# Optimization experiments

Measured on AMD Instinct MI355X. Metric: run time of the kernel, lower is better.

Reference implementation:

```python
import jax, jax.numpy as jnp
import numpy as np

L, B, T, V, E, H = 6, 4, 1024, 32000, 768, 12
D = E // H  # head_size = 64


def setup_inputs() -> dict:
    key = jax.random.key(0)
    ks = jax.random.split(key, 12)
    s = 0.02
    n = lambda k, shape: jax.random.normal(k, shape, jnp.float32) * s
    return {
        "idx": jax.random.randint(ks[0], (B, T), 0, V),
        "tok_emb": n(ks[1], (V, E)),
        "pos_emb": n(ks[2], (T, E)),
        "ln1_w": jnp.ones((L, E)), "ln1_b": jnp.zeros((L, E)),
        "wq": n(ks[3], (L, E, H, D)),
        "wk": n(ks[4], (L, E, H, D)),
        "wv": n(ks[5], (L, E, H, D)),
        "wo": n(ks[6], (L, E, E)), "bo": jnp.zeros((L, E)),
        "ln2_w": jnp.ones((L, E)), "ln2_b": jnp.zeros((L, E)),
        "w1": n(ks[7], (L, E, 4 * E)), "b1": jnp.zeros((L, 4 * E)),
        "w2": n(ks[8], (L, 4 * E, E)), "b2": jnp.zeros((L, E)),
        "lnf_w": jnp.ones((E,)), "lnf_b": jnp.zeros((E,)),
        "head_w": n(ks[9], (E, V)), "head_b": jnp.zeros((V,)),
    }


def _ln(x, w, b, eps=1e-5):
    m = x.mean(-1, keepdims=True)
    v = ((x - m) ** 2).mean(-1, keepdims=True)
    return (x - m) * jax.lax.rsqrt(v + eps) * w + b


def _forward(idx, tok_emb, pos_emb, ln1_w, ln1_b, wq, wk, wv, wo, bo,
             ln2_w, ln2_b, w1, b1, w2, b2, lnf_w, lnf_b, head_w, head_b):
    t = idx.shape[1]
    x = tok_emb[idx] + pos_emb[None, :t]          # [B,T,E]
    causal = jnp.tril(jnp.ones((t, t), bool))     # tril buffer
    scale = jnp.asarray(D, x.dtype) ** -0.5       # k.shape[-1] ** -0.5

    def block(x, p):
        l1w, l1b, Wq, Wk, Wv, Wo, Bo, l2w, l2b, W1, B1, W2, B2 = p
        h = _ln(x, l1w, l1b)
        q = jnp.einsum('btc,chd->bthd', h, Wq)
        k = jnp.einsum('btc,chd->bthd', h, Wk)
        v = jnp.einsum('btc,chd->bthd', h, Wv)
        wei = jnp.einsum('bqhd,bkhd->bhqk', q, k) * scale
        wei = jnp.where(causal, wei, -jnp.inf)
        wei = jax.nn.softmax(wei, axis=-1)
        att = jnp.einsum('bhqk,bkhd->bqhd', wei, v).reshape(x.shape)
        x = x + (att @ Wo + Bo)
        h2 = _ln(x, l2w, l2b)
        x = x + (jax.nn.relu(h2 @ W1 + B1) @ W2 + B2)
        return x, None

    params = (ln1_w, ln1_b, wq, wk, wv, wo, bo, ln2_w, ln2_b, w1, b1, w2, b2)
    x, _ = jax.lax.scan(block, x, params)
    x = _ln(x, lnf_w, lnf_b)
    return x @ head_w + head_b                    # [B,T,V] logits


def reference(idx, tok_emb, pos_emb, ln1_w, ln1_b, wq, wk, wv, wo, bo,
              ln2_w, ln2_b, w1, b1, w2, b2, lnf_w, lnf_b, head_w, head_b):
    return _forward(idx, tok_emb, pos_emb, ln1_w, ln1_b, wq, wk, wv, wo, bo,
                    ln2_w, ln2_b, w1, b1, w2, b2, lnf_w, lnf_b, head_w, head_b)
```

## Files before the change

### kernel.cpp

```cpp
#include <hip/hip_runtime.h>
#include <hip/hip_bf16.h>
#include <math.h>

#define L_LAYERS 6
#define BB 4
#define TT 1024
#define VV 32000
#define EE 768
#define HH 12
#define DD 64
#define BT (BB * TT)

typedef unsigned short u16;
typedef unsigned int   u32;
typedef __attribute__((ext_vector_type(8))) short short8;
typedef __attribute__((ext_vector_type(8))) unsigned short ushort8v;
typedef __attribute__((ext_vector_type(4))) float f32x4;

__device__ __forceinline__ float b2f_lo(u32 u) { union { u32 i; float f; } c; c.i = u << 16;          return c.f; }
__device__ __forceinline__ float b2f_hi(u32 u) { union { u32 i; float f; } c; c.i = u & 0xffff0000u;  return c.f; }
__device__ __forceinline__ u16  f2b(float f)   { union { float f; u32 i; } c{f}; u32 r = c.i + 0x7fffu + ((c.i >> 16) & 1u); return (u16)(r >> 16); }

__device__ __forceinline__ void gload16(const void* g, void* l) {
    __builtin_amdgcn_global_load_lds(
        (const __attribute__((address_space(1))) void*)g,
        (__attribute__((address_space(3))) void*)l, 16, 0, 0);
}

__global__ __launch_bounds__(256) void embed_kernel(
    const int* __restrict__ idx, const float* __restrict__ tok_emb,
    const float* __restrict__ pos_emb, float* __restrict__ x)
{
    int i = blockIdx.x * 256 + threadIdx.x;
    int e  = i % EE;
    int bt = i / EE;
    int t  = bt % TT;
    int tok = idx[bt];
    x[i] = tok_emb[(size_t)tok * EE + e] + pos_emb[(size_t)t * EE + e];
}

__global__ __launch_bounds__(256) void ln_kernel(
    const float* __restrict__ X, const float* __restrict__ w,
    const float* __restrict__ b, u16* __restrict__ Y)
{
    const int tid = threadIdx.x;
    const size_t row = blockIdx.x;
    const float* x = X + row * EE;

    float v0 = x[tid], v1 = x[tid + 256], v2 = x[tid + 512];

    __shared__ float red[256];
    red[tid] = v0 + v1 + v2;
    __syncthreads();
    for (int off = 128; off > 0; off >>= 1) {
        if (tid < off) red[tid] += red[tid + off];
        __syncthreads();
    }
    float mean = red[0] * (1.0f / EE);
    __syncthreads();
    float d0 = v0 - mean, d1 = v1 - mean, d2 = v2 - mean;
    red[tid] = d0 * d0 + d1 * d1 + d2 * d2;
    __syncthreads();
    for (int off = 128; off > 0; off >>= 1) {
        if (tid < off) red[tid] += red[tid + off];
        __syncthreads();
    }
    float rstd = rsqrtf(red[0] * (1.0f / EE) + 1e-5f);

    u16* y = Y + row * EE;
    y[tid]       = f2b(d0 * rstd * w[tid]       + b[tid]);
    y[tid + 256] = f2b(d1 * rstd * w[tid + 256] + b[tid + 256]);
    y[tid + 512] = f2b(d2 * rstd * w[tid + 512] + b[tid + 512]);
}

__device__ __forceinline__ void transpose_tile(
    const float* __restrict__ W, u16* __restrict__ Wt,
    int K, int N, int kt, int nt)
{
    __shared__ float t[32][33];
    const int k0 = kt * 32;
    const int n0 = nt * 32;
    const int c = threadIdx.x & 31;
    const int r = threadIdx.x >> 5;
    #pragma unroll
    for (int i = 0; i < 4; i++)
        t[r + i * 8][c] = W[(size_t)(k0 + r + i * 8) * N + n0 + c];
    __syncthreads();
    #pragma unroll
    for (int i = 0; i < 4; i++) {
        int rr = r + i * 8;
        Wt[(size_t)(n0 + rr) * K + k0 + c] = f2b(t[c][rr]);
    }
}

__global__ __launch_bounds__(256) void transpose_cvt(
    const float* __restrict__ W, u16* __restrict__ Wt, int K, int N)
{
    transpose_tile(W, Wt, K, N, blockIdx.y, blockIdx.x);
}

__global__ __launch_bounds__(256) void transpose_layer(
    const float* __restrict__ wq, const float* __restrict__ wk,
    const float* __restrict__ wv, const float* __restrict__ wo,
    const float* __restrict__ w1, const float* __restrict__ w2,
    u16* __restrict__ wt)
{
    const int t = blockIdx.x;
    if (t < 2304) {
        const int m = t / 576, r = t % 576;
        const float* Ws[4] = {wq, wk, wv, wo};
        transpose_tile(Ws[m], wt + (size_t)m * 768 * 768, 768, 768, r / 24, r % 24);
    } else if (t < 4608) {
        const int r = t - 2304;
        transpose_tile(w1, wt + (size_t)4 * 768 * 768, 768, 3072, r / 96, r % 96);
    } else {
        const int r = t - 4608;
        transpose_tile(w2, wt + (size_t)4 * 768 * 768 + (size_t)3072 * 768,
                       3072, 768, r / 24, r % 24);
    }
}

template<int RELU, int RES, int OUTBF, int MFRAG, int VECST>
__global__ __launch_bounds__(256) void gemm_bf16(
    const u16* __restrict__ A, const u16* __restrict__ Bt,
    const float* __restrict__ bias, const float* __restrict__ res,
    void* __restrict__ Cv, int M, int N, int K)
{
    constexpr int TM = MFRAG * 32;
    __shared__ u16 SH[(TM + 128) * 64];
    u16* As = SH;
    u16* Bs = SH + TM * 64;

    const int tid  = threadIdx.x;
    const int lane = tid & 63;
    const int w    = tid >> 6;
    const int wr   = w >> 1, wc = w & 1;
    const int m0 = blockIdx.x * TM;
    const int n0 = blockIdx.y * 128;

    const int cs = (lane & 7) ^ (lane >> 3);
    const int rl = lane >> 3;

    int aoff[2 * MFRAG], boff[8];
    const int kq = lane >> 4;
    #pragma unroll
    for (int mi = 0; mi < MFRAG; mi++) {
        int rg = wr * (MFRAG * 16) + mi * 16 + (lane & 15);
        #pragma unroll
        for (int ks = 0; ks < 2; ks++)
            aoff[2 * mi + ks] = rg * 64 + (((ks * 4 + kq) ^ (rg & 7)) * 8);
    }
    #pragma unroll
    for (int ni = 0; ni < 4; ni++) {
        int rg = wc * 64 + ni * 16 + (lane & 15);
        #pragma unroll
        for (int ks = 0; ks < 2; ks++)
            boff[2 * ni + ks] = rg * 64 + (((ks * 4 + kq) ^ (rg & 7)) * 8);
    }

    f32x4 acc[MFRAG][4] = {};

    for (int k0 = 0; k0 < K; k0 += 64) {
        __syncthreads();
        #pragma unroll
        for (int i = 0; i < MFRAG; i++) {
            const int seg = i * 4 + w;
            const int row = seg * 8 + rl;
            gload16(A + (size_t)(m0 + row) * K + k0 + cs * 8, &As[seg * 512]);
        }
        #pragma unroll
        for (int i = 0; i < 4; i++) {
            const int seg = i * 4 + w;
            const int row = seg * 8 + rl;
            gload16(Bt + (size_t)(n0 + row) * K + k0 + cs * 8, &Bs[seg * 512]);
        }
        __syncthreads();
        #pragma unroll
        for (int ks = 0; ks < 2; ks++) {
            short8 af[MFRAG], bfv[4];
            #pragma unroll
            for (int mi = 0; mi < MFRAG; mi++) af[mi] = *(const short8*)&As[aoff[2 * mi + ks]];
            #pragma unroll
            for (int ni = 0; ni < 4; ni++) bfv[ni] = *(const short8*)&Bs[boff[2 * ni + ks]];
            #pragma unroll
            for (int mi = 0; mi < MFRAG; mi++)
                #pragma unroll
                for (int ni = 0; ni < 4; ni++)
                    acc[mi][ni] = __builtin_amdgcn_mfma_f32_16x16x32_bf16(
                        af[mi], bfv[ni], acc[mi][ni], 0, 0, 0);
        }
    }

    const int rbase = m0 + wr * (MFRAG * 16) + (lane >> 4) * 4;
    const int cbase = n0 + wc * 64 + (lane & 15);

    if (VECST) {
        __syncthreads();
        float* CF = (float*)SH;
        #pragma unroll
        for (int ch = 0; ch < 2; ++ch) {
            if (wr == ch) {
                #pragma unroll
                for (int ni = 0; ni < 4; ni++) {
                    const int c = cbase + ni * 16;
                    const float bvf = bias ? bias[c] : 0.0f;
                    #pragma unroll
                    for (int mi = 0; mi < MFRAG; mi++)
                        #pragma unroll
                        for (int i = 0; i < 4; i++)
                            CF[(mi * 16 + kq * 4 + i) * 128 + wc * 64 + ni * 16 + (lane & 15)]
                                = acc[mi][ni][i] + bvf;
                }
            }
            __syncthreads();
            const int rr = tid >> 5;
            const int cc = (tid & 31) * 4;
            #pragma unroll
            for (int j = 0; j < 8; ++j) {
                const int r = rr + j * 8;
                *(f32x4*)&((float*)Cv)[(size_t)(m0 + ch * 64 + r) * N + n0 + cc]
                    = *(const f32x4*)&CF[r * 128 + cc];
            }
            if (ch == 0) __syncthreads();
        }
    } else {
        #pragma unroll
        for (int ni = 0; ni < 4; ni++) {
            const int c = cbase + ni * 16;
            const float bv = bias ? bias[c] : 0.0f;
            #pragma unroll
            for (int mi = 0; mi < MFRAG; mi++) {
                const int r = rbase + mi * 16;
                #pragma unroll
                for (int i = 0; i < 4; i++) {
                    float v = acc[mi][ni][i] + bv;
                    const size_t off = (size_t)(r + i) * N + c;
                    if (RES)  v += res[off];
                    if (RELU) v = fmaxf(v, 0.0f);
                    if (OUTBF) ((u16*)Cv)[off] = f2b(v);
                    else       ((float*)Cv)[off] = v;
                }
            }
        }
    }
}

#define AST 72
__global__ __launch_bounds__(256) void attn_mfma(
    const u16* __restrict__ qkv, u16* __restrict__ O)
{
    const int tid = threadIdx.x;
    const int qi = blockIdx.x;
    const int h  = blockIdx.y;
    const int b  = blockIdx.z;
    const int q0 = qi * 64;

    __shared__ u16 Ks[2][64 * 64];
    __shared__ u16 Vt[2][64 * AST];
    __shared__ u16 Ps[64 * AST];

    const int lane = tid & 63;
    const int w    = tid >> 6;
    const int lr   = lane & 15;
    const int lk   = lane >> 4;

    const int cs = (lane & 7) ^ (lane >> 3);
    const int rl = lane >> 3;
    const int vk2 = tid & 31;
    const int vdc = tid >> 5;

    {
        const int sr = tid >> 2, sc = tid & 3;
        const u16* src = qkv + (size_t)(b * TT + q0 + sr) * 2304 + h * 64 + sc * 16;
        *(ushort8v*)&Ps[sr * AST + sc * 16]     = *(const ushort8v*)src;
        *(ushort8v*)&Ps[sr * AST + sc * 16 + 8] = *(const ushort8v*)(src + 8);
    }
    __syncthreads();
    short8 aq[2];
    #pragma unroll
    for (int ks = 0; ks < 2; ks++)
        aq[ks] = *(const short8*)&Ps[(w * 16 + lr) * AST + lk * 8 + ks * 32];

    ushort8v vr0, vr1;
    auto K_ISSUE = [&](int t, int bf) {
        const int k0 = t * 64;
        #pragma unroll
        for (int j = 0; j < 2; ++j) {
            const int seg = j * 4 + w;
            const int row = seg * 8 + rl;
            gload16(qkv + (size_t)(b * TT + k0 + row) * 2304 + 768 + h * 64 + cs * 8,
                    &Ks[bf][seg * 512]);
        }
    };
    auto V_LOAD = [&](int t) {
        const int k0 = t * 64;
        const u16* p = qkv + (size_t)(b * TT + k0 + 2 * vk2) * 2304 + 1536 + h * 64 + vdc * 8;
        vr0 = *(const ushort8v*)p;
        vr1 = *(const ushort8v*)(p + 2304);
    };
    auto V_WRITE = [&](int bf) {
        #pragma unroll
        for (int j = 0; j < 8; ++j) {
            const u32 val = (u32)vr0[j] | ((u32)vr1[j] << 16);
            *(u32*)&Vt[bf][(vdc * 8 + j) * AST + 2 * vk2] = val;
        }
    };

    K_ISSUE(0, 0);
    V_LOAD(0);
    V_WRITE(0);
    __syncthreads();

    f32x4 oacc[4] = {};
    float m_run[4], l_run[4];
    #pragma unroll
    for (int i = 0; i < 4; i++) { m_run[i] = -3.0e38f; l_run[i] = 0.0f; }

    const int qrow = q0 + w * 16 + lk * 4;

    for (int t = 0; t <= qi; ++t) {
        const int cur = t & 1;

        f32x4 sfrag[4] = {};
        #pragma unroll
        for (int ks = 0; ks < 2; ks++)
            #pragma unroll
            for (int nt = 0; nt < 4; nt++) {
                const int rg = nt * 16 + lr;
                short8 bk = *(const short8*)&Ks[cur][rg * 64 + (((ks * 4 + lk) ^ (rg & 7)) * 8)];
                sfrag[nt] = __builtin_amdgcn_mfma_f32_16x16x32_bf16(aq[ks], bk, sfrag[nt], 0, 0, 0);
            }

        if (t < qi) { K_ISSUE(t + 1, cur ^ 1); V_LOAD(t + 1); }

        const int k0 = t * 64;
        float sv[4][4], mxv[4];
        float need = 0.0f;
        #pragma unroll
        for (int i = 0; i < 4; i++) {
            float mx = -3.0e38f;
            #pragma unroll
            for (int nt = 0; nt < 4; nt++) {
                float s = sfrag[nt][i] * 0.125f;
                if (t == qi && (k0 + nt * 16 + lr) > (qrow + i)) s = -3.0e38f;
                sv[i][nt] = s;
                mx = fmaxf(mx, s);
            }
            mx = fmaxf(mx, __shfl_xor(mx, 1));
            mx = fmaxf(mx, __shfl_xor(mx, 2));
            mx = fmaxf(mx, __shfl_xor(mx, 4));
            mx = fmaxf(mx, __shfl_xor(mx, 8));
            mxv[i] = mx;
            need = fmaxf(need, mx - m_run[i]);
        }
        if (!__all(need <= 8.0f)) {
            #pragma unroll
            for (int i = 0; i < 4; i++) {
                const float m_new = fmaxf(m_run[i], mxv[i]);
                const float scale = __expf(m_run[i] - m_new);
                l_run[i] *= scale;
                #pragma unroll
                for (int dt = 0; dt < 4; dt++) oacc[dt][i] *= scale;
                m_run[i] = m_new;
            }
        }
        #pragma unroll
        for (int i = 0; i < 4; i++) {
            float rs = 0.0f;
            #pragma unroll
            for (int nt = 0; nt < 4; nt++) {
                const float p = __expf(sv[i][nt] - m_run[i]);
                sv[i][nt] = p;
                rs += p;
            }
            rs += __shfl_xor(rs, 1);
            rs += __shfl_xor(rs, 2);
            rs += __shfl_xor(rs, 4);
            rs += __shfl_xor(rs, 8);
            l_run[i] += rs;
        }

        #pragma unroll
        for (int i = 0; i < 4; i++)
            #pragma unroll
            for (int nt = 0; nt < 4; nt++)
                Ps[(w * 16 + lk * 4 + i) * AST + nt * 16 + lr] = f2b(sv[i][nt]);

        #pragma unroll
        for (int ks = 0; ks < 2; ks++) {
            short8 ap = *(const short8*)&Ps[(w * 16 + lr) * AST + lk * 8 + ks * 32];
            #pragma unroll
            for (int dt = 0; dt < 4; dt++) {
                short8 bv = *(const short8*)&Vt[cur][(dt * 16 + lr) * AST + lk * 8 + ks * 32];
                oacc[dt] = __builtin_amdgcn_mfma_f32_16x16x32_bf16(ap, bv, oacc[dt], 0, 0, 0);
            }
        }

        if (t < qi) V_WRITE(cur ^ 1);
        __syncthreads();
    }

    #pragma unroll
    for (int i = 0; i < 4; i++) {
        const float inv = 1.0f / l_run[i];
        u16* dst = O + (size_t)(b * TT + q0 + w * 16 + lk * 4 + i) * 768 + h * 64 + lr;
        #pragma unroll
        for (int dt = 0; dt < 4; dt++)
            dst[dt * 16] = f2b(oacc[dt][i] * inv);
    }
}

extern "C" void kernel_launch(void* const* d_in, const int* in_sizes, int n_in,
                              void* d_out, int out_size, void* d_ws, size_t ws_size,
                              hipStream_t stream)
{
    (void)in_sizes; (void)n_in; (void)out_size; (void)ws_size;

    const int*   idx     = (const int*)  d_in[0];
    const float* tok_emb = (const float*)d_in[1];
    const float* pos_emb = (const float*)d_in[2];
    const float* ln1_w   = (const float*)d_in[3];
    const float* ln1_b   = (const float*)d_in[4];
    const float* wq      = (const float*)d_in[5];
    const float* wk      = (const float*)d_in[6];
    const float* wv      = (const float*)d_in[7];
    const float* wo      = (const float*)d_in[8];
    const float* bo      = (const float*)d_in[9];
    const float* ln2_w   = (const float*)d_in[10];
    const float* ln2_b   = (const float*)d_in[11];
    const float* w1      = (const float*)d_in[12];
    const float* b1      = (const float*)d_in[13];
    const float* w2      = (const float*)d_in[14];
    const float* b2      = (const float*)d_in[15];
    const float* lnf_w   = (const float*)d_in[16];
    const float* lnf_b   = (const float*)d_in[17];
    const float* head_w  = (const float*)d_in[18];
    const float* head_b  = (const float*)d_in[19];
    float* out = (float*)d_out;

    const size_t S = (size_t)BT * EE;
    float* x   = (float*)d_ws;
    u16*  qkv  = (u16*)(x + S);
    u16*  hb   = qkv + (size_t)BT * 2304;
    u16*  ffh  = hb + S;
    u16*  wt   = ffh + (size_t)BT * 3072;

    embed_kernel<<<BT * EE / 256, 256, 0, stream>>>(idx, tok_emb, pos_emb, x);

    for (int l = 0; l < L_LAYERS; l++) {
        const size_t oE  = (size_t)l * EE;
        const size_t oEE = (size_t)l * EE * EE;
        const size_t oEF = (size_t)l * EE * 4 * EE;

        transpose_layer<<<6912, 256, 0, stream>>>(
            wq + oEE, wk + oEE, wv + oEE, wo + oEE, w1 + oEF, w2 + oEF, wt);

        ln_kernel<<<BT, 256, 0, stream>>>(x, ln1_w + oE, ln1_b + oE, hb);
        gemm_bf16<0, 0, 1, 4, 0><<<dim3(BT / 128, 2304 / 128), 256, 0, stream>>>(
            hb, wt, nullptr, nullptr, qkv, BT, 2304, 768);
        attn_mfma<<<dim3(TT / 64, HH, BB), 256, 0, stream>>>(qkv, hb);
        gemm_bf16<0, 1, 0, 2, 0><<<dim3(BT / 64, 768 / 128), 256, 0, stream>>>(
            hb, wt + (size_t)3 * 768 * 768, bo + oE, x, x, BT, 768, 768);
        ln_kernel<<<BT, 256, 0, stream>>>(x, ln2_w + oE, ln2_b + oE, hb);
        gemm_bf16<1, 0, 1, 4, 0><<<dim3(BT / 128, 3072 / 128), 256, 0, stream>>>(
            hb, wt + (size_t)4 * 768 * 768, b1 + (size_t)l * 4 * EE, nullptr, ffh, BT, 3072, 768);
        gemm_bf16<0, 1, 0, 2, 0><<<dim3(BT / 64, 768 / 128), 256, 0, stream>>>(
            ffh, wt + (size_t)4 * 768 * 768 + (size_t)3072 * 768, b2 + oE, x, x, BT, 768, 3072);
    }

    ln_kernel<<<BT, 256, 0, stream>>>(x, lnf_w, lnf_b, hb);
    transpose_cvt<<<dim3(VV / 32, EE / 32), 256, 0, stream>>>(head_w, wt, EE, VV);
    gemm_bf16<0, 0, 0, 4, 1><<<dim3(BT / 128, VV / 128), 256, 0, stream>>>(
        hb, wt, head_b, nullptr, out, BT, VV, 768);
}
```

Baseline: 1.532 ms.

## Use wave-per-row layernorm, XCD-aware GEMM tile swizzle, exp2 softmax, drop staged store

```diff
diff --git a/kernel.cpp b/kernel.cpp
--- a/kernel.cpp
+++ b/kernel.cpp
@@ -15,6 +15,7 @@
 typedef unsigned int   u32;
 typedef __attribute__((ext_vector_type(8))) short short8;
 typedef __attribute__((ext_vector_type(8))) unsigned short ushort8v;
+typedef __attribute__((ext_vector_type(4))) unsigned short ushort4v;
 typedef __attribute__((ext_vector_type(4))) float f32x4;
 
 __device__ __forceinline__ float b2f_lo(u32 u) { union { u32 i; float f; } c; c.i = u << 16;          return c.f; }
@@ -43,34 +44,44 @@
     const float* __restrict__ X, const float* __restrict__ w,
     const float* __restrict__ b, u16* __restrict__ Y)
 {
-    const int tid = threadIdx.x;
-    const size_t row = blockIdx.x;
+    const int lane = threadIdx.x & 63;
+    const size_t row = blockIdx.x * 4 + (threadIdx.x >> 6);
     const float* x = X + row * EE;
 
-    float v0 = x[tid], v1 = x[tid + 256], v2 = x[tid + 512];
-
-    __shared__ float red[256];
-    red[tid] = v0 + v1 + v2;
-    __syncthreads();
-    for (int off = 128; off > 0; off >>= 1) {
-        if (tid < off) red[tid] += red[tid + off];
-        __syncthreads();
-    }
-    float mean = red[0] * (1.0f / EE);
-    __syncthreads();
-    float d0 = v0 - mean, d1 = v1 - mean, d2 = v2 - mean;
-    red[tid] = d0 * d0 + d1 * d1 + d2 * d2;
-    __syncthreads();
-    for (int off = 128; off > 0; off >>= 1) {
-        if (tid < off) red[tid] += red[tid + off];
-        __syncthreads();
-    }
-    float rstd = rsqrtf(red[0] * (1.0f / EE) + 1e-5f);
+    f32x4 v[3];
+    #pragma unroll
+    for (int k = 0; k < 3; k++)
+        v[k] = *(const f32x4*)&x[lane * 4 + k * 256];
+
+    float s = 0.0f;
+    #pragma unroll
+    for (int k = 0; k < 3; k++) s += v[k][0] + v[k][1] + v[k][2] + v[k][3];
+    #pragma unroll
+    for (int off = 32; off; off >>= 1) s += __shfl_xor(s, off);
+    const float mean = s * (1.0f / EE);
+
+    float q = 0.0f;
+    #pragma unroll
+    for (int k = 0; k < 3; k++)
+        #pragma unroll
+        for (int j = 0; j < 4; j++) {
+            v[k][j] -= mean;
+            q += v[k][j] * v[k][j];
+        }
+    #pragma unroll
+    for (int off = 32; off; off >>= 1) q += __shfl_xor(q, off);
+    const float rstd = rsqrtf(q * (1.0f / EE) + 1e-5f);
 
     u16* y = Y + row * EE;
-    y[tid]       = f2b(d0 * rstd * w[tid]       + b[tid]);
-    y[tid + 256] = f2b(d1 * rstd * w[tid + 256] + b[tid + 256]);
-    y[tid + 512] = f2b(d2 * rstd * w[tid + 512] + b[tid + 512]);
+    #pragma unroll
+    for (int k = 0; k < 3; k++) {
+        const f32x4 wv = *(const f32x4*)&w[lane * 4 + k * 256];
+        const f32x4 bv = *(const f32x4*)&b[lane * 4 + k * 256];
+        ushort4v o;
+        #pragma unroll
+        for (int j = 0; j < 4; j++) o[j] = f2b(v[k][j] * rstd * wv[j] + bv[j]);
+        *(ushort4v*)&y[lane * 4 + k * 256] = o;
+    }
 }
 
 __device__ __forceinline__ void transpose_tile(
@@ -120,23 +131,28 @@
     }
 }
 
-template<int RELU, int RES, int OUTBF, int MFRAG, int VECST>
+template<int RELU, int RES, int OUTBF, int MFRAG>
 __global__ __launch_bounds__(256) void gemm_bf16(
     const u16* __restrict__ A, const u16* __restrict__ Bt,
     const float* __restrict__ bias, const float* __restrict__ res,
     void* __restrict__ Cv, int M, int N, int K)
 {
     constexpr int TM = MFRAG * 32;
-    __shared__ u16 SH[(TM + 128) * 64];
-    u16* As = SH;
-    u16* Bs = SH + TM * 64;
+    __shared__ u16 As[TM * 64];
+    __shared__ u16 Bs[128 * 64];
 
     const int tid  = threadIdx.x;
     const int lane = tid & 63;
     const int w    = tid >> 6;
     const int wr   = w >> 1, wc = w & 1;
-    const int m0 = blockIdx.x * TM;
-    const int n0 = blockIdx.y * 128;
+
+    const int gx  = gridDim.x;
+    const int nwg = gx * gridDim.y;
+    const int lin = blockIdx.y * gx + blockIdx.x;
+    const int q8  = nwg >> 3;
+    const int s   = (lin & 7) * q8 + (lin >> 3);
+    const int m0  = (s % gx) * TM;
+    const int n0  = (s / gx) * 128;
 
     const int cs = (lane & 7) ^ (lane >> 3);
     const int rl = lane >> 3;
@@ -193,53 +209,21 @@
 
     const int rbase = m0 + wr * (MFRAG * 16) + (lane >> 4) * 4;
     const int cbase = n0 + wc * 64 + (lane & 15);
-
-    if (VECST) {
-        __syncthreads();
-        float* CF = (float*)SH;
-        #pragma unroll
-        for (int ch = 0; ch < 2; ++ch) {
-            if (wr == ch) {
-                #pragma unroll
-                for (int ni = 0; ni < 4; ni++) {
-                    const int c = cbase + ni * 16;
-                    const float bvf = bias ? bias[c] : 0.0f;
-                    #pragma unroll
-                    for (int mi = 0; mi < MFRAG; mi++)
-                        #pragma unroll
-                        for (int i = 0; i < 4; i++)
-                            CF[(mi * 16 + kq * 4 + i) * 128 + wc * 64 + ni * 16 + (lane & 15)]
-                                = acc[mi][ni][i] + bvf;
-                }
-            }
-            __syncthreads();
-            const int rr = tid >> 5;
-            const int cc = (tid & 31) * 4;
-            #pragma unroll
-            for (int j = 0; j < 8; ++j) {
-                const int r = rr + j * 8;
-                *(f32x4*)&((float*)Cv)[(size_t)(m0 + ch * 64 + r) * N + n0 + cc]
-                    = *(const f32x4*)&CF[r * 128 + cc];
-            }
-            if (ch == 0) __syncthreads();
-        }
-    } else {
-        #pragma unroll
-        for (int ni = 0; ni < 4; ni++) {
-            const int c = cbase + ni * 16;
-            const float bv = bias ? bias[c] : 0.0f;
-            #pragma unroll
-            for (int mi = 0; mi < MFRAG; mi++) {
-                const int r = rbase + mi * 16;
-                #pragma unroll
-                for (int i = 0; i < 4; i++) {
-                    float v = acc[mi][ni][i] + bv;
-                    const size_t off = (size_t)(r + i) * N + c;
-                    if (RES)  v += res[off];
-                    if (RELU) v = fmaxf(v, 0.0f);
-                    if (OUTBF) ((u16*)Cv)[off] = f2b(v);
-                    else       ((float*)Cv)[off] = v;
-                }
+    #pragma unroll
+    for (int ni = 0; ni < 4; ni++) {
+        const int c = cbase + ni * 16;
+        const float bv = bias ? bias[c] : 0.0f;
+        #pragma unroll
+        for (int mi = 0; mi < MFRAG; mi++) {
+            const int r = rbase + mi * 16;
+            #pragma unroll
+            for (int i = 0; i < 4; i++) {
+                float v = acc[mi][ni][i] + bv;
+                const size_t off = (size_t)(r + i) * N + c;
+                if (RES)  v += res[off];
+                if (RELU) v = fmaxf(v, 0.0f);
+                if (OUTBF) ((u16*)Cv)[off] = f2b(v);
+                else       ((float*)Cv)[off] = v;
             }
         }
     }
@@ -317,6 +301,7 @@
     for (int i = 0; i < 4; i++) { m_run[i] = -3.0e38f; l_run[i] = 0.0f; }
 
     const int qrow = q0 + w * 16 + lk * 4;
+    const float SC = 0.18033688f;
 
     for (int t = 0; t <= qi; ++t) {
         const int cur = t & 1;
@@ -341,7 +326,7 @@
             float mx = -3.0e38f;
             #pragma unroll
             for (int nt = 0; nt < 4; nt++) {
-                float s = sfrag[nt][i] * 0.125f;
+                float s = sfrag[nt][i] * SC;
                 if (t == qi && (k0 + nt * 16 + lr) > (qrow + i)) s = -3.0e38f;
                 sv[i][nt] = s;
                 mx = fmaxf(mx, s);
@@ -353,11 +338,11 @@
             mxv[i] = mx;
             need = fmaxf(need, mx - m_run[i]);
         }
-        if (!__all(need <= 8.0f)) {
+        if (!__all(need <= 11.5f)) {
             #pragma unroll
             for (int i = 0; i < 4; i++) {
                 const float m_new = fmaxf(m_run[i], mxv[i]);
-                const float scale = __expf(m_run[i] - m_new);
+                const float scale = exp2f(m_run[i] - m_new);
                 l_run[i] *= scale;
                 #pragma unroll
                 for (int dt = 0; dt < 4; dt++) oacc[dt][i] *= scale;
@@ -369,7 +354,7 @@
             float rs = 0.0f;
             #pragma unroll
             for (int nt = 0; nt < 4; nt++) {
-                const float p = __expf(sv[i][nt] - m_run[i]);
+                const float p = exp2f(sv[i][nt] - m_run[i]);
                 sv[i][nt] = p;
                 rs += p;
             }
@@ -455,21 +440,21 @@
         transpose_layer<<<6912, 256, 0, stream>>>(
             wq + oEE, wk + oEE, wv + oEE, wo + oEE, w1 + oEF, w2 + oEF, wt);
 
-        ln_kernel<<<BT, 256, 0, stream>>>(x, ln1_w + oE, ln1_b + oE, hb);
-        gemm_bf16<0, 0, 1, 4, 0><<<dim3(BT / 128, 2304 / 128), 256, 0, stream>>>(
+        ln_kernel<<<BT / 4, 256, 0, stream>>>(x, ln1_w + oE, ln1_b + oE, hb);
+        gemm_bf16<0, 0, 1, 4><<<dim3(BT / 128, 2304 / 128), 256, 0, stream>>>(
             hb, wt, nullptr, nullptr, qkv, BT, 2304, 768);
         attn_mfma<<<dim3(TT / 64, HH, BB), 256, 0, stream>>>(qkv, hb);
-        gemm_bf16<0, 1, 0, 2, 0><<<dim3(BT / 64, 768 / 128), 256, 0, stream>>>(
+        gemm_bf16<0, 1, 0, 2><<<dim3(BT / 64, 768 / 128), 256, 0, stream>>>(
             hb, wt + (size_t)3 * 768 * 768, bo + oE, x, x, BT, 768, 768);
-        ln_kernel<<<BT, 256, 0, stream>>>(x, ln2_w + oE, ln2_b + oE, hb);
-        gemm_bf16<1, 0, 1, 4, 0><<<dim3(BT / 128, 3072 / 128), 256, 0, stream>>>(
+        ln_kernel<<<BT / 4, 256, 0, stream>>>(x, ln2_w + oE, ln2_b + oE, hb);
+        gemm_bf16<1, 0, 1, 4><<<dim3(BT / 128, 3072 / 128), 256, 0, stream>>>(
             hb, wt + (size_t)4 * 768 * 768, b1 + (size_t)l * 4 * EE, nullptr, ffh, BT, 3072, 768);
-        gemm_bf16<0, 1, 0, 2, 0><<<dim3(BT / 64, 768 / 128), 256, 0, stream>>>(
+        gemm_bf16<0, 1, 0, 2><<<dim3(BT / 64, 768 / 128), 256, 0, stream>>>(
             ffh, wt + (size_t)4 * 768 * 768 + (size_t)3072 * 768, b2 + oE, x, x, BT, 768, 3072);
     }
 
-    ln_kernel<<<BT, 256, 0, stream>>>(x, lnf_w, lnf_b, hb);
+    ln_kernel<<<BT / 4, 256, 0, stream>>>(x, lnf_w, lnf_b, hb);
     transpose_cvt<<<dim3(VV / 32, EE / 32), 256, 0, stream>>>(head_w, wt, EE, VV);
-    gemm_bf16<0, 0, 0, 4, 1><<<dim3(BT / 128, VV / 128), 256, 0, stream>>>(
+    gemm_bf16<0, 0, 0, 4><<<dim3(BT / 128, VV / 128), 256, 0, stream>>>(
         hb, wt, head_b, nullptr, out, BT, VV, 768);
 }
```

Measured after the change: 1.555 ms. No clear change (+1.5%).
